# Kernel optimization log

Hardware: AMD Instinct MI355X
Metric: run time of the kernel (lower is better)

## Reference

```python
import jax, jax.numpy as jnp
import numpy as np

# Model constants (match init_kwargs)
DIMS = 4096
N_HEADS = 32
N_KV_HEADS = 8
HEAD_DIM = DIMS // N_HEADS          # 128
N_REP = N_HEADS // N_KV_HEADS       # 4
MAX_BSZ = 4
MAX_LEN = 2048
B, L = 4, 1024


def setup_inputs() -> dict:
    key = jax.random.key(0)
    ks = jax.random.split(key, 5)
    s = 0.02
    x = jax.random.normal(ks[0], (B, L, DIMS), jnp.float32)
    wq = jax.random.normal(ks[1], (DIMS, DIMS), jnp.float32) * s          # [out, in] like nn.Linear
    wk = jax.random.normal(ks[2], (N_KV_HEADS * HEAD_DIM, DIMS), jnp.float32) * s
    wv = jax.random.normal(ks[3], (N_KV_HEADS * HEAD_DIM, DIMS), jnp.float32) * s
    wo = jax.random.normal(ks[4], (DIMS, DIMS), jnp.float32) * s
    # RoPE angles: theta_i = pos / 10000^(2i/head_dim), shape [L, HEAD_DIM//2]
    inv_freq = 1.0 / (10000.0 ** (jnp.arange(0, HEAD_DIM, 2, dtype=jnp.float32) / HEAD_DIM))
    pos = jnp.arange(L, dtype=jnp.float32)
    freqs = pos[:, None] * inv_freq[None, :]
    # Additive causal mask [1, 1, L, L]
    mask = jnp.triu(jnp.full((1, 1, L, L), -1e9, jnp.float32), k=1)
    return {"x": x, "wq": wq, "wk": wk, "wv": wv, "wo": wo,
            "freqs": freqs, "mask": mask, "starting_pos": 0}


def _apply_rope(t, cos, sin):
    # t: [B, L, H, HEAD_DIM]; complex multiply on interleaved (even, odd) pairs
    tr = t.reshape(*t.shape[:-1], HEAD_DIM // 2, 2)
    a, b = tr[..., 0], tr[..., 1]
    out = jnp.stack([a * cos - b * sin, a * sin + b * cos], axis=-1)
    return out.reshape(t.shape)


def reference(x, wq, wk, wv, wo, freqs, mask, starting_pos):
    bsz, length, _ = x.shape
    hq = jnp.einsum('bld,ed->ble', x, wq).reshape(bsz, length, N_HEADS, HEAD_DIM)
    hk = jnp.einsum('bld,ed->ble', x, wk).reshape(bsz, length, N_KV_HEADS, HEAD_DIM)
    hv = jnp.einsum('bld,ed->ble', x, wv).reshape(bsz, length, N_KV_HEADS, HEAD_DIM)

    cos = jnp.cos(freqs)[None, :, None, :]   # [1, L, 1, HEAD_DIM//2]
    sin = jnp.sin(freqs)[None, :, None, :]
    hq = _apply_rope(hq, cos, sin)
    hk = _apply_rope(hk, cos, sin)

    # KV cache: write current k/v at starting_pos, read prefix [:starting_pos+length]
    cache_k = jnp.zeros((MAX_BSZ, MAX_LEN, N_KV_HEADS, HEAD_DIM), x.dtype)
    cache_v = jnp.zeros((MAX_BSZ, MAX_LEN, N_KV_HEADS, HEAD_DIM), x.dtype)
    cache_k = cache_k.at[:bsz, starting_pos:starting_pos + length].set(hk)
    cache_v = cache_v.at[:bsz, starting_pos:starting_pos + length].set(hv)
    k = cache_k[:bsz, :starting_pos + length]   # [B, S, KVH, HD]
    v = cache_v[:bsz, :starting_pos + length]

    # GQA: group queries by kv head instead of materializing repeated K/V
    q = hq.reshape(bsz, length, N_KV_HEADS, N_REP, HEAD_DIM)
    scores = jnp.einsum('blhrd,bshd->bhrls', q, k) / np.sqrt(HEAD_DIM).astype(x.dtype)
    scores = scores + mask[:, :, None, :, :]     # mask broadcast over rep dim
    probs = jax.nn.softmax(scores.astype(jnp.float32), axis=-1).astype(x.dtype)
    out = jnp.einsum('bhrls,bshd->blhrd', probs, v).reshape(bsz, length, DIMS)
    return jnp.einsum('bld,ed->ble', out, wo)
```

## Files before the change

### kernel.cpp

```cpp
#include <hip/hip_runtime.h>
#include <hip/hip_bf16.h>

typedef __attribute__((ext_vector_type(4))) float floatx4;
typedef __attribute__((ext_vector_type(8))) short short8;

static __device__ __forceinline__ float b2f(short s) {
    unsigned int u = ((unsigned int)(unsigned short)s) << 16;
    float f;
    __builtin_memcpy(&f, &u, 4);
    return f;
}
static __device__ __forceinline__ short f2b(float f) {
    __hip_bfloat16 h = __float2bfloat16(f);
    unsigned short u;
    __builtin_memcpy(&u, &h, 2);
    return (short)u;
}
static __device__ __forceinline__ void gll16(const void* g, void* l) {
    __builtin_amdgcn_global_load_lds(
        (const __attribute__((address_space(1))) unsigned int*)g,
        (__attribute__((address_space(3))) unsigned int*)l, 16, 0, 0);
}

__global__ void detect_dtype(const unsigned int* __restrict__ x, int off,
                             int* __restrict__ flag) {
    __shared__ int cnt[256];
    const int tid = threadIdx.x;
    const unsigned int w = x[off + tid];
    const unsigned int e = (w >> 7) & 0xFF;
    cnt[tid] = (e >= 110 && e <= 140) ? 1 : 0;
    __syncthreads();
    for (int s = 128; s > 0; s >>= 1) {
        if (tid < s) cnt[tid] += cnt[tid + s];
        __syncthreads();
    }
    if (tid == 0) *flag = (cnt[0] >= 160) ? 1 : 0;
}

__global__ __launch_bounds__(256) void to_bf16(const void* __restrict__ src,
                                               short* __restrict__ dst,
                                               const int* __restrict__ dflag,
                                               unsigned int n8) {
    const int isb = *dflag;
    const unsigned int i = blockIdx.x * 256 + threadIdx.x;
    if (i >= n8) return;
    const size_t e = (size_t)i * 8;
    if (isb) {
        *(short8*)(dst + e) = *(const short8*)((const short*)src + e);
    } else {
        const float4* sp = (const float4*)((const float*)src + e);
        const float4 f0 = sp[0], f1 = sp[1];
        short8 v;
        v[0] = f2b(f0.x); v[1] = f2b(f0.y); v[2] = f2b(f0.z); v[3] = f2b(f0.w);
        v[4] = f2b(f1.x); v[5] = f2b(f1.y); v[6] = f2b(f1.z); v[7] = f2b(f1.w);
        *(short8*)(dst + e) = v;
    }
}

#define QUAD_MFMA(MH, NH)                                                       \
    _Pragma("unroll") for (int i_ = 0; i_ < 4; ++i_)                            \
    _Pragma("unroll") for (int j_ = 0; j_ < 2; ++j_)                            \
    _Pragma("unroll") for (int kp_ = 0; kp_ < 2; ++kp_)                         \
        acc[(MH)*4 + i_][(NH)*2 + j_] = __builtin_amdgcn_mfma_f32_16x16x32_bf16(\
            aF[i_][kp_], bF[NH][j_][kp_], acc[(MH)*4 + i_][(NH)*2 + j_], 0, 0, 0);

#define READ_A(BUFP, MH)                                                        \
    _Pragma("unroll") for (int i_ = 0; i_ < 4; ++i_) {                          \
        const int r_ = (2 * i_ + wm) * 16 + l16;                                \
        _Pragma("unroll") for (int kp_ = 0; kp_ < 2; ++kp_)                     \
            aF[i_][kp_] = *(const short8*)&(BUFP)[(MH)*8192 + kp_*4096 + r_*32 + swzc]; \
    }

#define READ_B(BUFP, NH)                                                        \
    _Pragma("unroll") for (int j_ = 0; j_ < 2; ++j_) {                          \
        const int r_ = (4 * j_ + wn) * 16 + l16;                                \
        _Pragma("unroll") for (int kp_ = 0; kp_ < 2; ++kp_)                     \
            bF[NH][j_][kp_] = *(const short8*)&(BUFP)[16384 + (NH)*8192 + kp_*4096 + r_*32 + swzc]; \
    }

#define STAGE(BUFP, OPOFF, GBASE, ROW0, TT)                                     \
    {                                                                           \
        const short* g_ = (GBASE) + (size_t)((ROW0) + wave * 16 + (lane >> 2)) * K \
                          + (TT) * 64 + scol;                                   \
        gll16(g_, (BUFP) + (OPOFF) + wave * 512);                               \
        gll16(g_ + 32, (BUFP) + (OPOFF) + 4096 + wave * 512);                   \
    }

__global__ __launch_bounds__(512, 2) void gemm256(const short* __restrict__ A,
                                                  const short* __restrict__ B,
                                                  void* __restrict__ C,
                                                  int M, int N, int K,
                                                  const int* __restrict__ dflag,
                                                  int out_dyn) {
    __shared__ short lds[65536];
    const int isb = *dflag;
    const int tid = threadIdx.x;
    const int wave = tid >> 6, lane = tid & 63;
    const int wm = wave >> 2, wn = wave & 3;
    const int quad = lane >> 4, l16 = lane & 15;
    const int nwg = gridDim.x * gridDim.y;
    int lin = blockIdx.y * gridDim.x + blockIdx.x;
    lin = (lin & 7) * (nwg >> 3) + (lin >> 3);
    const int m0 = (lin / gridDim.x) * 256, n0 = (lin % gridDim.x) * 256;
    const int swzc = (quad * 8) ^ ((l16 & 8) << 1);
    const int scol = ((lane & 3) * 8) ^ (((lane >> 5) & 1) << 4);
    const int NG = K >> 6;

    floatx4 acc[8][4] = {};
    short8 aF[4][2], bF[2][2][2];

    {
        const int t1p = (1 < NG) ? 1 : NG - 1;
        STAGE(lds, 0, A, m0, 0);
        STAGE(lds, 16384, B, n0, 0);
        STAGE(lds, 16384 + 8192, B, n0 + 128, 0);
        STAGE(lds, 8192, A, m0 + 128, 0);
        STAGE(lds + 32768, 0, A, m0, t1p);
        STAGE(lds + 32768, 16384 + 8192, B, n0 + 128, t1p);
    }
    asm volatile("s_waitcnt vmcnt(4)" ::: "memory");
    __builtin_amdgcn_s_barrier();
    __builtin_amdgcn_sched_barrier(0);

    for (int g = 0; g < NG; ++g) {
        short* bufc = lds + (g & 1) * 32768;
        short* bufn = lds + ((g + 1) & 1) * 32768;
        const int t1 = (g + 1 < NG) ? g + 1 : NG - 1;
        const int t2 = (g + 2 < NG) ? g + 2 : NG - 1;
        READ_A(bufc, 0);
        READ_B(bufc, 0);
        STAGE(bufn, 8192, A, m0 + 128, t1);
        STAGE(bufn, 16384, B, n0, t1);
        __builtin_amdgcn_s_barrier();
        __builtin_amdgcn_s_setprio(1);
        QUAD_MFMA(0, 0);
        __builtin_amdgcn_s_setprio(0);
        __builtin_amdgcn_s_barrier();
        READ_B(bufc, 1);
        __builtin_amdgcn_s_barrier();
        __builtin_amdgcn_s_setprio(1);
        QUAD_MFMA(0, 1);
        __builtin_amdgcn_s_setprio(0);
        __builtin_amdgcn_s_barrier();
        READ_A(bufc, 1);
        STAGE(bufc, 0, A, m0, t2);
        __builtin_amdgcn_s_barrier();
        __builtin_amdgcn_s_setprio(1);
        QUAD_MFMA(1, 1);
        __builtin_amdgcn_s_setprio(0);
        __builtin_amdgcn_s_barrier();
        STAGE(bufc, 16384 + 8192, B, n0 + 128, t2);
        asm volatile("s_waitcnt vmcnt(4)" ::: "memory");
        __builtin_amdgcn_s_barrier();
        __builtin_amdgcn_sched_barrier(0);
        __builtin_amdgcn_s_setprio(1);
        QUAD_MFMA(1, 0);
        __builtin_amdgcn_s_setprio(0);
        __builtin_amdgcn_s_barrier();
    }
    asm volatile("s_waitcnt vmcnt(0)" ::: "memory");

#pragma unroll
    for (int i = 0; i < 8; ++i)
#pragma unroll
        for (int j = 0; j < 4; ++j)
#pragma unroll
            for (int rr = 0; rr < 4; ++rr) {
                const size_t row = m0 + (2 * i + wm) * 16 + quad * 4 + rr;
                const size_t col = n0 + (4 * j + wn) * 16 + l16;
                const float v = acc[i][j][rr];
                if (out_dyn && !isb)
                    ((float*)C)[row * N + col] = v;
                else
                    ((short*)C)[row * N + col] = f2b(v);
            }
}

__global__ __launch_bounds__(256) void gemm_bt_f(const short* __restrict__ A,
                                                 const void* __restrict__ B,
                                                 void* __restrict__ C,
                                                 int M, int N, int K,
                                                 const int* __restrict__ dflag,
                                                 int b_dyn, int out_dyn) {
    __shared__ short As[128 * 32];
    __shared__ short Bs[128 * 32];
    const int isb = *dflag;
    const int b_bf = b_dyn ? isb : 1;
    const int tid = threadIdx.x;
    const int wave = tid >> 6, lane = tid & 63;
    const int quad = lane >> 4, l16 = lane & 15;
    const int wm = (wave >> 1) * 64, wn = (wave & 1) * 64;
    const int m0 = blockIdx.y * 128, n0 = blockIdx.x * 128;
    const int g_r = lane >> 2;
    const int g_c = (lane & 3) * 8;
    const short* agp = A + (size_t)(m0 + wave * 32 + g_r) * K + g_c;
    const short* bgp = (const short*)B + (size_t)(n0 + wave * 32 + g_r) * K + g_c;
    short* const asl0 = &As[(wave * 32) * 32];
    short* const asl1 = &As[(wave * 32 + 16) * 32];
    short* const bsl0 = &Bs[(wave * 32) * 32];
    short* const bsl1 = &Bs[(wave * 32 + 16) * 32];
    const size_t kstep16 = (size_t)16 * K;
    const int s_r = tid >> 1, s_c = (tid & 1) * 16;
    const size_t brow_f = (size_t)(n0 + s_r) * K + s_c;

    floatx4 acc[4][4] = {};
    for (int k0 = 0; k0 < K; k0 += 32) {
        gll16(agp + k0, asl0);
        gll16(agp + k0 + kstep16, asl1);
        if (b_bf) {
            gll16(bgp + k0, bsl0);
            gll16(bgp + k0 + kstep16, bsl1);
        } else {
            const float* bp = (const float*)B + brow_f + k0;
            const float4 f0 = ((const float4*)bp)[0], f1 = ((const float4*)bp)[1];
            const float4 f2 = ((const float4*)bp)[2], f3 = ((const float4*)bp)[3];
            short8 v0, v1;
            v0[0] = f2b(f0.x); v0[1] = f2b(f0.y); v0[2] = f2b(f0.z); v0[3] = f2b(f0.w);
            v0[4] = f2b(f1.x); v0[5] = f2b(f1.y); v0[6] = f2b(f1.z); v0[7] = f2b(f1.w);
            v1[0] = f2b(f2.x); v1[1] = f2b(f2.y); v1[2] = f2b(f2.z); v1[3] = f2b(f2.w);
            v1[4] = f2b(f3.x); v1[5] = f2b(f3.y); v1[6] = f2b(f3.z); v1[7] = f2b(f3.w);
            *(short8*)&Bs[s_r * 32 + s_c] = v0;
            *(short8*)&Bs[s_r * 32 + s_c + 8] = v1;
        }
        __syncthreads();
        short8 af[4], bq[4];
#pragma unroll
        for (int i = 0; i < 4; i++)
            af[i] = *(const short8*)&As[(wm + i * 16 + l16) * 32 + quad * 8];
#pragma unroll
        for (int j = 0; j < 4; j++)
            bq[j] = *(const short8*)&Bs[(wn + j * 16 + l16) * 32 + quad * 8];
#pragma unroll
        for (int i = 0; i < 4; i++)
#pragma unroll
            for (int j = 0; j < 4; j++)
                acc[i][j] = __builtin_amdgcn_mfma_f32_16x16x32_bf16(af[i], bq[j], acc[i][j], 0, 0, 0);
        __syncthreads();
    }
#pragma unroll
    for (int i = 0; i < 4; i++)
#pragma unroll
        for (int j = 0; j < 4; j++)
#pragma unroll
            for (int rr = 0; rr < 4; rr++) {
                const size_t row = m0 + wm + i * 16 + quad * 4 + rr;
                const size_t col = n0 + wn + j * 16 + l16;
                const float v = acc[i][j][rr];
                if (out_dyn && !isb)
                    ((float*)C)[row * N + col] = v;
                else
                    ((short*)C)[row * N + col] = f2b(v);
            }
}

__global__ __launch_bounds__(256) void rope_kernel(short* __restrict__ Qb,
                                                   short* __restrict__ Kb,
                                                   const void* __restrict__ freqs,
                                                   const int* __restrict__ fflag) {
    const int isb = *fflag;
    const int idx = blockIdx.x * 256 + threadIdx.x;
    constexpr int QP = 4096 * 32 * 64;
    short* ptr;
    int t, p;
    if (idx < QP) {
        t = idx >> 11;
        const int rem = idx & 2047;
        p = rem & 63;
        ptr = Qb + (size_t)t * 4096 + (rem >> 6) * 128 + 2 * p;
    } else {
        const int i = idx - QP;
        t = i >> 9;
        const int rem = i & 511;
        p = rem & 63;
        ptr = Kb + (size_t)t * 2048 + (rem >> 6) * 128 + 2 * p;
    }
    const int fi = (t & 1023) * 64 + p;
    const float f = isb ? b2f(((const short*)freqs)[fi]) : ((const float*)freqs)[fi];
    float sv, cv;
    sincosf(f, &sv, &cv);
    const float a = b2f(ptr[0]);
    const float bb = b2f(ptr[1]);
    ptr[0] = f2b(a * cv - bb * sv);
    ptr[1] = f2b(a * sv + bb * cv);
}

__global__ __launch_bounds__(256) void attn_kernel(const short* __restrict__ Q,
                                                   const short* __restrict__ Kc,
                                                   const short* __restrict__ Vc,
                                                   short* __restrict__ AO) {
    constexpr int LQ = 136, LV = 72, LP = 72;
    __shared__ short Qs[64 * LQ];
    __shared__ short Ks[64 * LQ];
    __shared__ short Vts[128 * LV];
    __shared__ short Ps[64 * LP];
    const int tid = threadIdx.x;
    const int qt = blockIdx.x, h = blockIdx.y, b = blockIdx.z;
    const int kvh = h >> 2;
    const size_t tbase = (size_t)b * 1024;
    const int q0 = qt * 64;
    const int wave = tid >> 6, lane = tid & 63;
    const int quad = lane >> 4, l16 = lane & 15;
    const int sr = tid >> 2, sc = (tid & 3) * 32;
    {
        const short* src = Q + (tbase + q0 + sr) * 4096 + h * 128 + sc;
#pragma unroll
        for (int j = 0; j < 4; j++)
            *(short8*)&Qs[sr * LQ + sc + 8 * j] = *(const short8*)(src + 8 * j);
    }
    floatx4 o[8] = {};
    float mrow[4], lrow[4];
#pragma unroll
    for (int rr = 0; rr < 4; rr++) { mrow[rr] = -1.0e30f; lrow[rr] = 0.0f; }
    const float scale = 0.08838834764831845f;
    for (int kt = 0; kt <= qt; kt++) {
        if (kt > 0) __syncthreads();
        {
            const short* ksrc = Kc + (tbase + kt * 64 + sr) * 2048 + kvh * 128 + sc;
#pragma unroll
            for (int j = 0; j < 4; j++)
                *(short8*)&Ks[sr * LQ + sc + 8 * j] = *(const short8*)(ksrc + 8 * j);
            const short* vsrc = Vc + (tbase + kt * 64 + sr) * 2048 + kvh * 128 + sc;
            short vv[32];
#pragma unroll
            for (int j = 0; j < 4; j++)
                *(short8*)(vv + 8 * j) = *(const short8*)(vsrc + 8 * j);
#pragma unroll
            for (int e = 0; e < 32; e++)
                Vts[(sc + e) * LV + sr] = vv[e];
        }
        __syncthreads();
        short8 aq[4];
#pragma unroll
        for (int kk = 0; kk < 4; kk++)
            aq[kk] = *(const short8*)&Qs[(wave * 16 + l16) * LQ + kk * 32 + quad * 8];
        floatx4 s[4];
#pragma unroll
        for (int j = 0; j < 4; j++) {
            floatx4 acc = {};
#pragma unroll
            for (int kk = 0; kk < 4; kk++) {
                short8 bk = *(const short8*)&Ks[(j * 16 + l16) * LQ + kk * 32 + quad * 8];
                acc = __builtin_amdgcn_mfma_f32_16x16x32_bf16(aq[kk], bk, acc, 0, 0, 0);
            }
            s[j] = acc;
        }
        const int qrow = q0 + wave * 16 + quad * 4;
#pragma unroll
        for (int j = 0; j < 4; j++)
#pragma unroll
            for (int rr = 0; rr < 4; rr++) {
                const float v = s[j][rr] * scale;
                const int key = kt * 64 + j * 16 + l16;
                s[j][rr] = (key > qrow + rr) ? -1.0e9f : v;
            }
        float alpha[4];
#pragma unroll
        for (int rr = 0; rr < 4; rr++) {
            float mx = fmaxf(fmaxf(s[0][rr], s[1][rr]), fmaxf(s[2][rr], s[3][rr]));
#pragma unroll
            for (int off = 1; off < 16; off <<= 1)
                mx = fmaxf(mx, __shfl_xor(mx, off, 64));
            const float mnew = fmaxf(mrow[rr], mx);
            alpha[rr] = __expf(mrow[rr] - mnew);
            float rsum = 0.0f;
#pragma unroll
            for (int j = 0; j < 4; j++) {
                const float p = __expf(s[j][rr] - mnew);
                s[j][rr] = p;
                rsum += p;
            }
#pragma unroll
            for (int off = 1; off < 16; off <<= 1)
                rsum += __shfl_xor(rsum, off, 64);
            lrow[rr] = lrow[rr] * alpha[rr] + rsum;
            mrow[rr] = mnew;
        }
#pragma unroll
        for (int c = 0; c < 8; c++)
#pragma unroll
            for (int rr = 0; rr < 4; rr++)
                o[c][rr] *= alpha[rr];
#pragma unroll
        for (int j = 0; j < 4; j++)
#pragma unroll
            for (int rr = 0; rr < 4; rr++)
                Ps[(wave * 16 + quad * 4 + rr) * LP + j * 16 + l16] = f2b(s[j][rr]);
        __syncthreads();
        short8 ap[2];
        ap[0] = *(const short8*)&Ps[(wave * 16 + l16) * LP + quad * 8];
        ap[1] = *(const short8*)&Ps[(wave * 16 + l16) * LP + 32 + quad * 8];
#pragma unroll
        for (int c = 0; c < 8; c++) {
#pragma unroll
            for (int kk = 0; kk < 2; kk++) {
                short8 bv = *(const short8*)&Vts[(c * 16 + l16) * LV + kk * 32 + quad * 8];
                o[c] = __builtin_amdgcn_mfma_f32_16x16x32_bf16(ap[kk], bv, o[c], 0, 0, 0);
            }
        }
    }
    float invl[4];
#pragma unroll
    for (int rr = 0; rr < 4; rr++) invl[rr] = 1.0f / lrow[rr];
#pragma unroll
    for (int c = 0; c < 8; c++)
#pragma unroll
        for (int rr = 0; rr < 4; rr++) {
            const size_t row = tbase + q0 + wave * 16 + quad * 4 + rr;
            AO[row * 4096 + h * 128 + c * 16 + l16] = f2b(o[c][rr] * invl[rr]);
        }
}

extern "C" void kernel_launch(void* const* d_in, const int* in_sizes, int n_in,
                              void* d_out, int out_size, void* d_ws, size_t ws_size,
                              hipStream_t stream) {
    const void* x     = d_in[0];
    const void* wq    = d_in[1];
    const void* wk    = d_in[2];
    const void* wv    = d_in[3];
    const void* wo    = d_in[4];
    const void* freqs = d_in[5];
    char* ws = (char*)d_ws;
    int* flag = (int*)ws;
    short* KV = (short*)(ws + 256);
    short* WB = (short*)(ws + 256 + 16777216);
    short* AO = WB;
    short* WOB = (short*)(ws + 256 + 16777216 + 33554432);
    short* Qb = (short*)d_out;
    short* Xb = (short*)d_out + 16777216;
    const bool big_ws = ws_size >= (size_t)(256 + 16777216 + 33554432 + 33554432);

    detect_dtype<<<1, 256, 0, stream>>>((const unsigned int*)x, 0, flag);
    detect_dtype<<<1, 256, 0, stream>>>((const unsigned int*)freqs, 100, flag + 1);
    to_bf16<<<8192, 256, 0, stream>>>(x, Xb, flag, 2097152);
    to_bf16<<<8192, 256, 0, stream>>>(wq, WB, flag, 2097152);
    gemm256<<<dim3(16, 16), 512, 0, stream>>>(Xb, WB, Qb, 4096, 4096, 4096, flag, 0);
    to_bf16<<<2048, 256, 0, stream>>>(wk, WB, flag, 524288);
    to_bf16<<<2048, 256, 0, stream>>>(wv, WB + 4194304, flag, 524288);
    gemm256<<<dim3(8, 16), 512, 0, stream>>>(Xb, WB, KV, 4096, 2048, 4096, flag, 0);
    rope_kernel<<<40960, 256, 0, stream>>>(Qb, KV, freqs, flag + 1);
    attn_kernel<<<dim3(16, 32, 4), 256, 0, stream>>>(Qb, KV, KV + 1024, AO);
    if (big_ws) {
        to_bf16<<<8192, 256, 0, stream>>>(wo, WOB, flag, 2097152);
        gemm256<<<dim3(16, 16), 512, 0, stream>>>(AO, WOB, d_out, 4096, 4096, 4096, flag, 1);
    } else {
        gemm_bt_f<<<dim3(32, 32), 256, 0, stream>>>(AO, wo, d_out, 4096, 4096, 4096, flag, 1, 1);
    }
}
```

Baseline: 816.1 us.

## Pre-transpose V, precompute RoPE LUT, and stream K/V from global in attention

A separate kernel writes V transposed into scratch, and a small LUT kernel precomputes cos/sin once. The RoPE kernel is vectorized to 8 elements per thread and folds the softmax scale into Q. The attention kernel drops its Q/K/V shared-memory staging and block barriers, reading K and transposed V fragments straight from global memory. It also reverses the query-tile order so the heaviest causal tiles launch first. This removes LDS transposes and barriers, but every wave now re-reads K/V from global or cache instead of sharing them through LDS.

Result: slower. 1.036 ms (+27.0%).

```diff
diff --git a/kernel.cpp b/kernel.cpp
--- a/kernel.cpp
+++ b/kernel.cpp
@@ -253,93 +253,112 @@
             }
 }
 
+__global__ __launch_bounds__(256) void transpose_v(const short* __restrict__ KV,
+                                                   short* __restrict__ Vt) {
+    __shared__ short Ts[64 * 136];
+    const int tid = threadIdx.x;
+    const int t0 = blockIdx.x * 64;
+    const int kvh = blockIdx.y, b = blockIdx.z;
+    const int sr = tid >> 2, sc = (tid & 3) * 32;
+    const short* src = KV + (size_t)(b * 1024 + t0 + sr) * 2048 + 1024 + kvh * 128 + sc;
+#pragma unroll
+    for (int j = 0; j < 4; ++j)
+        *(short8*)&Ts[sr * 136 + sc + 8 * j] = *(const short8*)(src + 8 * j);
+    __syncthreads();
+    short* dst = Vt + (size_t)(b * 8 + kvh) * 128 * 1024 + t0;
+#pragma unroll
+    for (int p = 0; p < 4; ++p) {
+        const int d = p * 32 + (tid >> 3);
+        const int tk = (tid & 7) * 8;
+        short8 v;
+#pragma unroll
+        for (int e = 0; e < 8; ++e) v[e] = Ts[(tk + e) * 136 + d];
+        *(short8*)(dst + (size_t)d * 1024 + tk) = v;
+    }
+}
+
+__global__ __launch_bounds__(256) void rope_lut(const void* __restrict__ freqs,
+                                                const int* __restrict__ fflag,
+                                                float2* __restrict__ cs) {
+    const int isb = *fflag;
+    const int i = blockIdx.x * 256 + threadIdx.x;
+    const float f = isb ? b2f(((const short*)freqs)[i]) : ((const float*)freqs)[i];
+    float sv, cv;
+    __sincosf(f, &sv, &cv);
+    cs[i] = make_float2(cv, sv);
+}
+
 __global__ __launch_bounds__(256) void rope_kernel(short* __restrict__ Qb,
                                                    short* __restrict__ Kb,
-                                                   const void* __restrict__ freqs,
-                                                   const int* __restrict__ fflag) {
-    const int isb = *fflag;
-    const int idx = blockIdx.x * 256 + threadIdx.x;
-    constexpr int QP = 4096 * 32 * 64;
-    short* ptr;
-    int t, p;
-    if (idx < QP) {
-        t = idx >> 11;
-        const int rem = idx & 2047;
-        p = rem & 63;
-        ptr = Qb + (size_t)t * 4096 + (rem >> 6) * 128 + 2 * p;
+                                                   const float2* __restrict__ cs) {
+    const int g = blockIdx.x * 256 + threadIdx.x;
+    constexpr int QG = 4096 * 512;
+    short* base;
+    int t, gp;
+    float qs;
+    if (g < QG) {
+        t = g >> 9;
+        const int rem = g & 511;
+        gp = rem & 15;
+        base = Qb + (size_t)t * 4096 + (rem >> 4) * 128 + gp * 8;
+        qs = 0.08838834764831845f;
     } else {
-        const int i = idx - QP;
-        t = i >> 9;
-        const int rem = i & 511;
-        p = rem & 63;
-        ptr = Kb + (size_t)t * 2048 + (rem >> 6) * 128 + 2 * p;
-    }
-    const int fi = (t & 1023) * 64 + p;
-    const float f = isb ? b2f(((const short*)freqs)[fi]) : ((const float*)freqs)[fi];
-    float sv, cv;
-    sincosf(f, &sv, &cv);
-    const float a = b2f(ptr[0]);
-    const float bb = b2f(ptr[1]);
-    ptr[0] = f2b(a * cv - bb * sv);
-    ptr[1] = f2b(a * sv + bb * cv);
+        const int i = g - QG;
+        t = i >> 7;
+        const int rem = i & 127;
+        gp = rem & 15;
+        base = Kb + (size_t)t * 2048 + (rem >> 4) * 128 + gp * 8;
+        qs = 1.0f;
+    }
+    const int fi0 = (t & 1023) * 64 + gp * 4;
+    short8 v = *(const short8*)base;
+    short8 r;
+#pragma unroll
+    for (int j = 0; j < 4; ++j) {
+        const float2 c = cs[fi0 + j];
+        const float a = b2f(v[2 * j]);
+        const float bb = b2f(v[2 * j + 1]);
+        r[2 * j]     = f2b((a * c.x - bb * c.y) * qs);
+        r[2 * j + 1] = f2b((a * c.y + bb * c.x) * qs);
+    }
+    *(short8*)base = r;
 }
 
 __global__ __launch_bounds__(256) void attn_kernel(const short* __restrict__ Q,
                                                    const short* __restrict__ Kc,
-                                                   const short* __restrict__ Vc,
+                                                   const short* __restrict__ Vt,
                                                    short* __restrict__ AO) {
-    constexpr int LQ = 136, LV = 72, LP = 72;
-    __shared__ short Qs[64 * LQ];
-    __shared__ short Ks[64 * LQ];
-    __shared__ short Vts[128 * LV];
+    constexpr int LP = 72;
     __shared__ short Ps[64 * LP];
     const int tid = threadIdx.x;
-    const int qt = blockIdx.x, h = blockIdx.y, b = blockIdx.z;
+    const int qt = gridDim.x - 1 - blockIdx.x;
+    const int h = blockIdx.y, b = blockIdx.z;
     const int kvh = h >> 2;
     const size_t tbase = (size_t)b * 1024;
     const int q0 = qt * 64;
     const int wave = tid >> 6, lane = tid & 63;
     const int quad = lane >> 4, l16 = lane & 15;
-    const int sr = tid >> 2, sc = (tid & 3) * 32;
+    short8 aq[4];
     {
-        const short* src = Q + (tbase + q0 + sr) * 4096 + h * 128 + sc;
-#pragma unroll
-        for (int j = 0; j < 4; j++)
-            *(short8*)&Qs[sr * LQ + sc + 8 * j] = *(const short8*)(src + 8 * j);
-    }
+        const short* qp = Q + (tbase + q0 + wave * 16 + l16) * 4096 + h * 128 + quad * 8;
+#pragma unroll
+        for (int kk = 0; kk < 4; ++kk) aq[kk] = *(const short8*)(qp + kk * 32);
+    }
+    const short* kb = Kc + tbase * 2048 + (size_t)kvh * 128 + quad * 8;
+    const short* vb = Vt + ((size_t)(b * 8 + kvh) * 128 + l16) * 1024 + quad * 8;
     floatx4 o[8] = {};
     float mrow[4], lrow[4];
 #pragma unroll
     for (int rr = 0; rr < 4; rr++) { mrow[rr] = -1.0e30f; lrow[rr] = 0.0f; }
-    const float scale = 0.08838834764831845f;
     for (int kt = 0; kt <= qt; kt++) {
-        if (kt > 0) __syncthreads();
-        {
-            const short* ksrc = Kc + (tbase + kt * 64 + sr) * 2048 + kvh * 128 + sc;
-#pragma unroll
-            for (int j = 0; j < 4; j++)
-                *(short8*)&Ks[sr * LQ + sc + 8 * j] = *(const short8*)(ksrc + 8 * j);
-            const short* vsrc = Vc + (tbase + kt * 64 + sr) * 2048 + kvh * 128 + sc;
-            short vv[32];
-#pragma unroll
-            for (int j = 0; j < 4; j++)
-                *(short8*)(vv + 8 * j) = *(const short8*)(vsrc + 8 * j);
-#pragma unroll
-            for (int e = 0; e < 32; e++)
-                Vts[(sc + e) * LV + sr] = vv[e];
-        }
-        __syncthreads();
-        short8 aq[4];
-#pragma unroll
-        for (int kk = 0; kk < 4; kk++)
-            aq[kk] = *(const short8*)&Qs[(wave * 16 + l16) * LQ + kk * 32 + quad * 8];
         floatx4 s[4];
 #pragma unroll
         for (int j = 0; j < 4; j++) {
             floatx4 acc = {};
 #pragma unroll
             for (int kk = 0; kk < 4; kk++) {
-                short8 bk = *(const short8*)&Ks[(j * 16 + l16) * LQ + kk * 32 + quad * 8];
+                const short8 bk = *(const short8*)(kb +
+                    (size_t)(kt * 64 + j * 16 + l16) * 2048 + kk * 32);
                 acc = __builtin_amdgcn_mfma_f32_16x16x32_bf16(aq[kk], bk, acc, 0, 0, 0);
             }
             s[j] = acc;
@@ -349,9 +368,8 @@
         for (int j = 0; j < 4; j++)
 #pragma unroll
             for (int rr = 0; rr < 4; rr++) {
-                const float v = s[j][rr] * scale;
                 const int key = kt * 64 + j * 16 + l16;
-                s[j][rr] = (key > qrow + rr) ? -1.0e9f : v;
+                s[j][rr] = (key > qrow + rr) ? -1.0e9f : s[j][rr];
             }
         float alpha[4];
 #pragma unroll
@@ -380,12 +398,15 @@
 #pragma unroll
             for (int rr = 0; rr < 4; rr++)
                 o[c][rr] *= alpha[rr];
+        asm volatile("s_waitcnt lgkmcnt(0)" ::: "memory");
+        __builtin_amdgcn_sched_barrier(0);
 #pragma unroll
         for (int j = 0; j < 4; j++)
 #pragma unroll
             for (int rr = 0; rr < 4; rr++)
                 Ps[(wave * 16 + quad * 4 + rr) * LP + j * 16 + l16] = f2b(s[j][rr]);
-        __syncthreads();
+        asm volatile("s_waitcnt lgkmcnt(0)" ::: "memory");
+        __builtin_amdgcn_sched_barrier(0);
         short8 ap[2];
         ap[0] = *(const short8*)&Ps[(wave * 16 + l16) * LP + quad * 8];
         ap[1] = *(const short8*)&Ps[(wave * 16 + l16) * LP + 32 + quad * 8];
@@ -393,7 +414,8 @@
         for (int c = 0; c < 8; c++) {
 #pragma unroll
             for (int kk = 0; kk < 2; kk++) {
-                short8 bv = *(const short8*)&Vts[(c * 16 + l16) * LV + kk * 32 + quad * 8];
+                const short8 bv = *(const short8*)(vb +
+                    (size_t)(c * 16) * 1024 + kt * 64 + kk * 32);
                 o[c] = __builtin_amdgcn_mfma_f32_16x16x32_bf16(ap[kk], bv, o[c], 0, 0, 0);
             }
         }
@@ -427,6 +449,8 @@
     short* WOB = (short*)(ws + 256 + 16777216 + 33554432);
     short* Qb = (short*)d_out;
     short* Xb = (short*)d_out + 16777216;
+    short* Vtb = (short*)d_out + 16777216;
+    float2* cs = (float2*)((char*)d_out + 33554432 + 8388608);
     const bool big_ws = ws_size >= (size_t)(256 + 16777216 + 33554432 + 33554432);
 
     detect_dtype<<<1, 256, 0, stream>>>((const unsigned int*)x, 0, flag);
@@ -437,8 +461,10 @@
     to_bf16<<<2048, 256, 0, stream>>>(wk, WB, flag, 524288);
     to_bf16<<<2048, 256, 0, stream>>>(wv, WB + 4194304, flag, 524288);
     gemm256<<<dim3(8, 16), 512, 0, stream>>>(Xb, WB, KV, 4096, 2048, 4096, flag, 0);
-    rope_kernel<<<40960, 256, 0, stream>>>(Qb, KV, freqs, flag + 1);
-    attn_kernel<<<dim3(16, 32, 4), 256, 0, stream>>>(Qb, KV, KV + 1024, AO);
+    transpose_v<<<dim3(16, 8, 4), 256, 0, stream>>>(KV, Vtb);
+    rope_lut<<<256, 256, 0, stream>>>(freqs, flag + 1, cs);
+    rope_kernel<<<10240, 256, 0, stream>>>(Qb, KV, cs);
+    attn_kernel<<<dim3(16, 32, 4), 256, 0, stream>>>(Qb, KV, Vtb, AO);
     if (big_ws) {
         to_bf16<<<8192, 256, 0, stream>>>(wo, WOB, flag, 2097152);
         gemm256<<<dim3(16, 16), 512, 0, stream>>>(AO, WOB, d_out, 4096, 4096, 4096, flag, 1);
```
